# Performance work log

Measured on AMD Instinct MI355X. Metric: run time of the kernel, lower is better.

The kernel has to match this reference:

```python
import jax, jax.numpy as jnp
import numpy as np

K = 7        # upsample_kernel_size
S = 2        # upscale_factor
EK = K - 2   # encoder kernel size (5)


def conv2d(x, w, b, padding):
    out = jax.lax.conv_general_dilated(
        x, w, window_strides=(1, 1), padding=[(padding, padding), (padding, padding)],
        dimension_numbers=('NCHW', 'OIHW', 'NCHW'))
    return out + b[None, :, None, None]


def pixel_shuffle(x, s):
    B, C, H, W = x.shape
    oc = C // (s * s)
    x = x.reshape(B, oc, s, s, H, W)
    x = x.transpose(0, 1, 4, 2, 5, 3)
    return x.reshape(B, oc, H * s, W * s)


def carafe(x, kmap, k, s):
    # x: [B,C,H,W], kmap: [B,k*k,H*s,W*s] softmax-normalized
    B, C, H, W = x.shape
    pad = k // 2
    xp = jnp.pad(x, ((0, 0), (0, 0), (pad, pad), (pad, pad)))
    # k^2 shifted views -> [B,C,k2,H,W]
    patches = jnp.stack([xp[:, :, dy:dy + H, dx:dx + W]
                         for dy in range(k) for dx in range(k)], axis=2)
    # output pixel (i,j) reads source (i//s, j//s): factor kmap spatial dims
    km = kmap.reshape(B, k * k, H, s, W, s)
    out = jnp.einsum('bcnhw,bnhpwq->bchpwq', patches, km)
    return out.reshape(B, C, H * s, W * s)


def setup_inputs() -> dict:
    key = jax.random.key(0)
    k1, k2, k3 = jax.random.split(key, 3)
    B, C, H, W = 4, 256, 64, 64
    comp_c = 64
    enc_out = (S * K) ** 2  # 196
    x = jax.random.normal(k1, (B, C, H, W), dtype=jnp.float32)
    w_comp = jax.random.normal(k2, (comp_c, C, 1, 1), dtype=jnp.float32) * (1.0 / np.sqrt(C))
    b_comp = jnp.zeros((comp_c,), dtype=jnp.float32)
    w_enc = jax.random.normal(k3, (enc_out, comp_c, EK, EK), dtype=jnp.float32) * (1.0 / np.sqrt(comp_c * EK * EK))
    b_enc = jnp.zeros((enc_out,), dtype=jnp.float32)
    return {'x': x, 'w_comp': w_comp, 'b_comp': b_comp, 'w_enc': w_enc, 'b_enc': b_enc}


def reference(x, w_comp, b_comp, w_enc, b_enc):
    compressed = conv2d(x, w_comp, b_comp, padding=0)
    content = conv2d(compressed, w_enc, b_enc, padding=EK // 2)
    upsampled = pixel_shuffle(content, S)            # [B, k^2, H*s, W*s]
    kernel_map = jax.nn.softmax(upsampled, axis=1)
    return carafe(x, kernel_map, K, S)
```

## Files before the change

### kernel.cpp

```cpp
#include <hip/hip_runtime.h>
#include <math.h>
#include <stdint.h>

#define B_   4
#define C_   256
#define H_   64
#define W_   64
#define CC_  64
#define OE_  196
#define OH_  128
#define OW_  128
#define XH_  72
#define NWB_ 10

typedef uint32_t u32;
typedef unsigned short u16;
typedef __attribute__((ext_vector_type(8))) short bf16x8;
typedef __attribute__((ext_vector_type(4))) float f32x4;
typedef __attribute__((ext_vector_type(4))) u32 u32x4;
typedef __attribute__((ext_vector_type(2))) u32 u32x2;

__device__ __forceinline__ u16 f2bf(float f) {
  u32 u = __builtin_bit_cast(u32, f);
  u32 r = (u + 0x7FFFu + ((u >> 16) & 1u)) >> 16;
  return (u16)r;
}

__global__ __launch_bounds__(256) void prep_weights(
    const float* __restrict__ w_comp, const float* __restrict__ w_enc,
    u16* __restrict__ wfrag, u16* __restrict__ wcf,
    u16* __restrict__ xw8) {
  int idx = blockIdx.x * 256 + threadIdx.x;
  if (idx < 50 * 14 * 64) {
    int lane = idx & 63;
    int mt   = (idx >> 6) % 14;
    int ks   = idx / (14 * 64);
    int o    = mt * 16 + (lane & 15);
    int tap  = ks >> 1, s = ks & 1;
    int ky   = tap / 5, kx = tap % 5;
    int cb   = s * 32 + (lane >> 4) * 8;
    u32 pk[4];
    #pragma unroll
    for (int p = 0; p < 4; ++p) {
      u16 lo = 0, hi = 0;
      if (o < OE_) {
        lo = f2bf(w_enc[((o * CC_ + cb + 2 * p) * 5 + ky) * 5 + kx]);
        hi = f2bf(w_enc[((o * CC_ + cb + 2 * p + 1) * 5 + ky) * 5 + kx]);
      }
      pk[p] = (u32)lo | ((u32)hi << 16);
    }
    *reinterpret_cast<u32x4*>(wfrag + (size_t)idx * 8) =
        *reinterpret_cast<u32x4*>(pk);
  }
  if (idx < 8 * 4 * 64) {
    int lane = idx & 63;
    int mt   = (idx >> 6) & 3;
    int ks   = idx >> 8;
    int o    = mt * 16 + (lane & 15);
    int cb   = ks * 32 + (lane >> 4) * 8;
    u32 pk[4];
    #pragma unroll
    for (int p = 0; p < 4; ++p) {
      u16 lo = f2bf(w_comp[o * C_ + cb + 2 * p]);
      u16 hi = f2bf(w_comp[o * C_ + cb + 2 * p + 1]);
      pk[p] = (u32)lo | ((u32)hi << 16);
    }
    *reinterpret_cast<u32x4*>(wcf + (size_t)idx * 8) =
        *reinterpret_cast<u32x4*>(pk);
  }
  {
    u32x4 z = {0, 0, 0, 0};
    for (int i = idx; i < 1088 * 256; i += 65536) {
      int zi = i >> 8, ck = i & 255;
      int b = zi / 272, r = zi % 272;
      int hp, wb;
      if (r < 30)      { hp = r / 10;             wb = r % 10; }
      else if (r < 80) { hp = 67 + (r - 30) / 10; wb = (r - 30) % 10; }
      else {
        int rr = r - 80;
        hp = 3 + rr / 3;
        int m = rr % 3;
        wb = (m == 0) ? 0 : (m == 1) ? 8 : 9;
      }
      *reinterpret_cast<u32x4*>(
          xw8 + (((size_t)(b * XH_ + hp)) * NWB_ + wb) * (C_ * 8) + ck * 8) = z;
    }
  }
}

__global__ __launch_bounds__(256) void compress_k(
    const float* __restrict__ x, const u16* __restrict__ wcf,
    const float* __restrict__ b_comp, u16* __restrict__ comp,
    u16* __restrict__ xw8) {
  __shared__ float xs[C_ * 20];
  int t   = threadIdx.x;
  int gid = blockIdx.x;
  int wq  = gid & 3;
  int bh  = gid >> 2;
  int b = bh >> 6, h = bh & 63;
  int w0 = wq * 16;

  const float* xrow = x + (size_t)b * C_ * H_ * W_ + (size_t)h * W_ + w0;
  for (int i = t; i < 1024; i += 256) {
    int c = i >> 2, q = i & 3;
    f32x4 v = *reinterpret_cast<const f32x4*>(xrow + (size_t)c * H_ * W_ + q * 4);
    *reinterpret_cast<f32x4*>(xs + c * 20 + q * 4) = v;
  }
  __syncthreads();

  int wv   = __builtin_amdgcn_readfirstlane(t >> 6);
  int lane = t & 63;
  int w    = lane & 15;
  int lg   = lane >> 4;

  bf16x8 af[8];
  #pragma unroll
  for (int ks = 0; ks < 8; ++ks)
    af[ks] = *reinterpret_cast<const bf16x8*>(
        wcf + (((size_t)ks * 4 + wv) * 64 + lane) * 8);

  f32x4 acc = {0.f, 0.f, 0.f, 0.f};
  #pragma unroll
  for (int ks = 0; ks < 8; ++ks) {
    short vv[8];
    #pragma unroll
    for (int j = 0; j < 8; ++j)
      vv[j] = (short)f2bf(xs[(ks * 32 + lg * 8 + j) * 20 + w]);
    bf16x8 bf = (bf16x8){vv[0], vv[1], vv[2], vv[3], vv[4], vv[5], vv[6], vv[7]};
    acc = __builtin_amdgcn_mfma_f32_16x16x32_bf16(af[ks], bf, acc, 0, 0, 0);
  }

  {
    int cc0 = wv * 16 + lg * 4;
    f32x4 bias = *reinterpret_cast<const f32x4*>(b_comp + cc0);
    u32 p0 = (u32)f2bf(acc[0] + bias[0]) | ((u32)f2bf(acc[1] + bias[1]) << 16);
    u32 p1 = (u32)f2bf(acc[2] + bias[2]) | ((u32)f2bf(acc[3] + bias[3]) << 16);
    u32x2 pk = {p0, p1};
    *reinterpret_cast<u32x2*>(comp + ((size_t)bh * 64 + w0 + w) * CC_ + cc0) = pk;
  }

  {
    int ww = t & 15, cq = t >> 4;
    int wp = w0 + ww + 3;
    size_t base = (((size_t)(b * XH_ + h + 3)) * NWB_ + (wp >> 3)) * (C_ * 8) + (wp & 7);
    #pragma unroll
    for (int i = 0; i < 16; ++i) {
      int c = cq * 16 + i;
      xw8[base + c * 8] = f2bf(xs[c * 20 + ww]);
    }
  }
}

#define ELG_ 32256

__device__ __forceinline__ void enc_lda(
    bf16x8 (&a)[2], const u16* __restrict__ wfrag,
    int ks, int mtbase, int lane) {
  #pragma unroll
  for (int mm = 0; mm < 2; ++mm)
    a[mm] = *reinterpret_cast<const bf16x8*>(
        wfrag + (((size_t)ks * 14 + mtbase + mm) * 64 + lane) * 8);
}

__device__ __forceinline__ void enc_step(
    int ks, const char* lds, const bf16x8 (&a)[2], f32x4 (&acc)[2][2],
    int nlane, int kq) {
  int tap = ks >> 1, s = ks & 1;
  int ky = tap / 5, kx = tap % 5;
  bf16x8 bf[2];
  #pragma unroll
  for (int nt = 0; nt < 2; ++nt) {
    int col = nt * 16 + nlane + kx;
    int byte = (((ky * 36 + col) * 64 + s * 32 + kq * 8) * 2) ^ ((col & 7) << 4);
    bf[nt] = *reinterpret_cast<const bf16x8*>(lds + byte);
  }
  #pragma unroll
  for (int mm = 0; mm < 2; ++mm)
    #pragma unroll
    for (int nt = 0; nt < 2; ++nt)
      acc[mm][nt] = __builtin_amdgcn_mfma_f32_16x16x32_bf16(
          a[mm], bf[nt], acc[mm][nt], 0, 0, 0);
}

__global__ __launch_bounds__(512) void enc_mfma_k(
    const u16* __restrict__ comp, const u16* __restrict__ wfrag,
    const float* __restrict__ b_enc, u16* __restrict__ bfrB) {
  __shared__ __align__(16) char lds[ELG_];

  int t   = threadIdx.x;
  int bid = blockIdx.x;
  int swz = (bid & 7) * 64 + (bid >> 3);
  int wh  = swz & 1;
  int bh  = swz >> 1;
  int b = bh >> 6, h = bh & 63;
  int w0 = wh * 32;

  {
    const u16* cbse = comp + (size_t)b * H_ * W_ * CC_;
    for (int i = t; i < 1440; i += 512) {
      int q = i & 7, colr = i >> 3;
      int col = colr % 36, r = colr / 36;
      int hh = h - 2 + r, gw = w0 - 2 + col;
      u32x4 v = {0, 0, 0, 0};
      if ((unsigned)hh < H_ && (unsigned)gw < W_)
        v = *reinterpret_cast<const u32x4*>(cbse + ((size_t)hh * W_ + gw) * CC_ + q * 8);
      int byte = ((r * 36 + col) * 128 + q * 16) ^ ((col & 7) << 4);
      *reinterpret_cast<u32x4*>(lds + byte) = v;
    }
  }
  __syncthreads();

  int wv    = __builtin_amdgcn_readfirstlane(t >> 6);
  int lane  = t & 63;
  int nlane = lane & 15, kq = lane >> 4;
  int mtbase = wv * 2;

  f32x4 acc[2][2];
  #pragma unroll
  for (int mm = 0; mm < 2; ++mm)
    #pragma unroll
    for (int nt = 0; nt < 2; ++nt) acc[mm][nt] = (f32x4){0.f, 0.f, 0.f, 0.f};

  if (wv < 7) {
    bf16x8 abuf[4][2];
    #pragma unroll
    for (int p = 0; p < 4; ++p) enc_lda(abuf[p], wfrag, p, mtbase, lane);
    #pragma unroll
    for (int ks = 0; ks < 50; ++ks) {
      enc_step(ks, lds, abuf[ks & 3], acc, nlane, kq);
      if (ks < 46) enc_lda(abuf[ks & 3], wfrag, ks + 4, mtbase, lane);
    }
  }

  __syncthreads();
  float* lg = (float*)lds;
  if (wv < 7) {
    #pragma unroll
    for (int mm = 0; mm < 2; ++mm) {
      #pragma unroll
      for (int nt = 0; nt < 2; ++nt) {
        #pragma unroll
        for (int r = 0; r < 4; ++r) {
          int m  = (mtbase + mm) * 16 + kq * 4 + r;
          int px = nt * 16 + nlane;
          lg[m * 36 + px] = acc[mm][nt][r] + (m < OE_ ? b_enc[m] : 0.f);
        }
      }
    }
  }
  __syncthreads();

  float v[49];
  float inv = 0.f;
  if (t < 128) {
    int px = t & 31, rr = t >> 5;
    float mx = -1e30f;
    #pragma unroll
    for (int n = 0; n < 49; ++n) {
      v[n] = lg[(4 * n + rr) * 36 + px];
      mx = fmaxf(mx, v[n]);
    }
    float sum = 0.f;
    #pragma unroll
    for (int n = 0; n < 49; ++n) { v[n] = __expf(v[n] - mx); sum += v[n]; }
    inv = 1.f / sum;
  }
  __syncthreads();

  if (t < 128) {
    int px = t & 31, rr = t >> 5;
    u16* sva = (u16*)lds;
    int myo = (px * 4 + rr) * 49;
    #pragma unroll
    for (int n = 0; n < 49; ++n) sva[myo + n] = f2bf(v[n] * inv);

    int wi = px & 7, wg = wh * 4 + (px >> 3);
    int p = rr >> 1, q = rr & 1;
    size_t bb = ((((size_t)(b * 64 + h) * 8 + wg) * 2 + p) * 4) * 512 +
                (size_t)(wi * 2 + q) * 8;
    #pragma unroll
    for (int ks = 0; ks < 4; ++ks) {
      #pragma unroll
      for (int lg2 = 0; lg2 < 4; ++lg2) {
        u32 pk[4];
        #pragma unroll
        for (int jp = 0; jp < 4; ++jp) {
          u16 e[2];
          #pragma unroll
          for (int u = 0; u < 2; ++u) {
            int j  = jp * 2 + u;
            int k  = ks * 32 + lg2 * 8 + j;
            int dy = k >> 4, dxp = k & 15;
            int dx = dxp - wi;
            bool ok = (dy < 7) && (dx >= 0) && (dx < 7);
            int idx = ok ? (dy * 7 + dx) : 0;
            u16 s = sva[myo + idx];
            e[u] = ok ? s : (u16)0;
          }
          pk[jp] = (u32)e[0] | ((u32)e[1] << 16);
        }
        *reinterpret_cast<u32x4*>(bfrB + bb + (size_t)ks * 512 + lg2 * 128) =
            *reinterpret_cast<u32x4*>(pk);
      }
    }
  }
}

__device__ __forceinline__ void carafe_lda(
    bf16x8 (&buf)[4], const u16* __restrict__ xb,
    int c, int h, int wg, int lg) {
  #pragma unroll
  for (int ks = 0; ks < 4; ++ks) {
    int dy = ks * 2 + (lg >> 1);
    buf[ks] = *reinterpret_cast<const bf16x8*>(
        xb + (((size_t)(h + dy)) * NWB_ + wg + (lg & 1)) * (C_ * 8) + c * 8);
  }
}

__global__ __launch_bounds__(256) void carafe_k(
    const u16* __restrict__ xw8, const u16* __restrict__ bfrB,
    float* __restrict__ out) {
  int t   = threadIdx.x;
  int bid = blockIdx.x;
  int swz = (bid & 7) * 256 + (bid >> 3);
  int mh  = swz & 1;
  int wgp = (swz >> 1) & 3;
  int h   = (swz >> 3) & 63;
  int b   = swz >> 9;

  int wv   = t >> 6;
  int lane = t & 63;
  int wg   = wgp * 2 + (wv & 1);
  int mq   = wv >> 1;
  int mt0  = mh * 8 + mq * 4;
  int col  = lane & 15;
  int lg   = lane >> 4;
  int mrow = lane & 15;
  int w0   = wg * 8;

  bf16x8 bfp[2][4];
  size_t bbase = (((size_t)(b * 64 + h) * 8 + wg) * 2) * 4 * 512;
  #pragma unroll
  for (int p = 0; p < 2; ++p)
    #pragma unroll
    for (int ks = 0; ks < 4; ++ks)
      bfp[p][ks] = *reinterpret_cast<const bf16x8*>(
          bfrB + bbase + (size_t)(p * 4 + ks) * 512 + lane * 8);

  const u16* xb = xw8 + (size_t)b * XH_ * NWB_ * (C_ * 8);
  bf16x8 bufA[4], bufB[4];
  carafe_lda(bufA, xb, mt0 * 16 + mrow, h, wg, lg);

  #pragma unroll
  for (int i = 0; i < 4; ++i) {
    int mt = mt0 + i;
    if (i < 3) {
      if (i & 1) carafe_lda(bufA, xb, (mt + 1) * 16 + mrow, h, wg, lg);
      else       carafe_lda(bufB, xb, (mt + 1) * 16 + mrow, h, wg, lg);
    }
    f32x4 acc0 = {0.f, 0.f, 0.f, 0.f};
    f32x4 acc1 = {0.f, 0.f, 0.f, 0.f};
    #pragma unroll
    for (int ks = 0; ks < 4; ++ks) {
      bf16x8 af = (i & 1) ? bufB[ks] : bufA[ks];
      acc0 = __builtin_amdgcn_mfma_f32_16x16x32_bf16(af, bfp[0][ks], acc0, 0, 0, 0);
      acc1 = __builtin_amdgcn_mfma_f32_16x16x32_bf16(af, bfp[1][ks], acc1, 0, 0, 0);
    }
    float* o0 = out +
        ((size_t)(b * C_ + mt * 16 + lg * 4) * OH_ + 2 * h) * OW_ + 2 * w0 + col;
    o0[0]                     = acc0[0];
    o0[(size_t)OH_ * OW_]     = acc0[1];
    o0[2 * (size_t)OH_ * OW_] = acc0[2];
    o0[3 * (size_t)OH_ * OW_] = acc0[3];
    float* o1 = o0 + OW_;
    o1[0]                     = acc1[0];
    o1[(size_t)OH_ * OW_]     = acc1[1];
    o1[2 * (size_t)OH_ * OW_] = acc1[2];
    o1[3 * (size_t)OH_ * OW_] = acc1[3];
  }
}

extern "C" void kernel_launch(void* const* d_in, const int* in_sizes, int n_in,
                              void* d_out, int out_size, void* d_ws, size_t ws_size,
                              hipStream_t stream) {
  const float* x      = (const float*)d_in[0];
  const float* w_comp = (const float*)d_in[1];
  const float* b_comp = (const float*)d_in[2];
  const float* w_enc  = (const float*)d_in[3];
  const float* b_enc  = (const float*)d_in[4];
  float* out = (float*)d_out;

  u16* bfrB  = (u16*)d_ws;
  u16* wfrag = bfrB + 8388608;
  u16* wcf   = wfrag + 358400;
  u16* comp  = wcf + 16384;
  u16* xw8   = comp + 1048576;

  prep_weights<<<256, 256, 0, stream>>>(w_comp, w_enc, wfrag, wcf, xw8);
  compress_k<<<B_ * H_ * 4, 256, 0, stream>>>(x, wcf, b_comp, comp, xw8);
  enc_mfma_k<<<512, 512, 0, stream>>>(comp, wfrag, b_enc, bfrB);
  carafe_k<<<2048, 256, 0, stream>>>(xw8, bfrB, out);
}
```

Baseline: 65.68 us.

## Realign compress blocks to 8-wide padded tiles and write xw8 with 16-byte stores

Compress blocks now cover a window shifted by the 3-pixel halo padding, so each block fills two whole 8-pixel groups of the padded bf16 x layout. Those groups are written with one 16-byte vector store per channel instead of 16 scattered 2-byte stores per thread. The side halo columns are written by the compress kernel itself (as zeros from the masked loads), which leaves prep_weights only the top and bottom rows to zero. The cost is one extra block per row (5 instead of 4), which recomputes some columns and masks their output, plus unaligned scalar LDS stores.

```diff
diff --git a/kernel.cpp b/kernel.cpp
--- a/kernel.cpp
+++ b/kernel.cpp
@@ -70,18 +70,11 @@
   }
   {
     u32x4 z = {0, 0, 0, 0};
-    for (int i = idx; i < 1088 * 256; i += 65536) {
-      int zi = i >> 8, ck = i & 255;
-      int b = zi / 272, r = zi % 272;
-      int hp, wb;
-      if (r < 30)      { hp = r / 10;             wb = r % 10; }
-      else if (r < 80) { hp = 67 + (r - 30) / 10; wb = (r - 30) % 10; }
-      else {
-        int rr = r - 80;
-        hp = 3 + rr / 3;
-        int m = rr % 3;
-        wb = (m == 0) ? 0 : (m == 1) ? 8 : 9;
-      }
+    for (int i = idx; i < 81920; i += 65536) {
+      int ck = i & 255, zi = i >> 8;
+      int b = zi / 80, r = zi % 80;
+      int hp8 = r / 10, wb = r % 10;
+      int hp = (hp8 < 3) ? hp8 : 64 + hp8;
       *reinterpret_cast<u32x4*>(
           xw8 + (((size_t)(b * XH_ + hp)) * NWB_ + wb) * (C_ * 8) + ck * 8) = z;
     }
@@ -92,25 +85,29 @@
     const float* __restrict__ x, const u16* __restrict__ wcf,
     const float* __restrict__ b_comp, u16* __restrict__ comp,
     u16* __restrict__ xw8) {
-  __shared__ float xs[C_ * 20];
+  __shared__ float xs[C_ * 25];
   int t   = threadIdx.x;
   int gid = blockIdx.x;
-  int wq  = gid & 3;
-  int bh  = gid >> 2;
+  int wq  = gid % 5;
+  int bh  = gid / 5;
   int b = bh >> 6, h = bh & 63;
-  int w0 = wq * 16;
-
-  const float* xrow = x + (size_t)b * C_ * H_ * W_ + (size_t)h * W_ + w0;
-  for (int i = t; i < 1024; i += 256) {
-    int c = i >> 2, q = i & 3;
-    f32x4 v = *reinterpret_cast<const f32x4*>(xrow + (size_t)c * H_ * W_ + q * 4);
-    *reinterpret_cast<f32x4*>(xs + c * 20 + q * 4) = v;
+  int wbase = wq * 16 - 4;
+
+  const float* xrow = x + (size_t)b * C_ * H_ * W_ + (size_t)h * W_;
+  for (int i = t; i < 1280; i += 256) {
+    int c = i / 5, q = i - (i / 5) * 5;
+    int gw0 = wbase + q * 4;
+    f32x4 v = {0.f, 0.f, 0.f, 0.f};
+    if ((unsigned)gw0 < 61u)
+      v = *reinterpret_cast<const f32x4*>(xrow + (size_t)c * H_ * W_ + gw0);
+    float* r = xs + c * 25 + q * 4;
+    r[0] = v[0]; r[1] = v[1]; r[2] = v[2]; r[3] = v[3];
   }
   __syncthreads();
 
   int wv   = __builtin_amdgcn_readfirstlane(t >> 6);
   int lane = t & 63;
-  int w    = lane & 15;
+  int i16  = lane & 15;
   int lg   = lane >> 4;
 
   bf16x8 af[8];
@@ -125,28 +122,38 @@
     short vv[8];
     #pragma unroll
     for (int j = 0; j < 8; ++j)
-      vv[j] = (short)f2bf(xs[(ks * 32 + lg * 8 + j) * 20 + w]);
+      vv[j] = (short)f2bf(xs[(ks * 32 + lg * 8 + j) * 25 + i16 + 1]);
     bf16x8 bf = (bf16x8){vv[0], vv[1], vv[2], vv[3], vv[4], vv[5], vv[6], vv[7]};
     acc = __builtin_amdgcn_mfma_f32_16x16x32_bf16(af[ks], bf, acc, 0, 0, 0);
   }
 
   {
-    int cc0 = wv * 16 + lg * 4;
-    f32x4 bias = *reinterpret_cast<const f32x4*>(b_comp + cc0);
-    u32 p0 = (u32)f2bf(acc[0] + bias[0]) | ((u32)f2bf(acc[1] + bias[1]) << 16);
-    u32 p1 = (u32)f2bf(acc[2] + bias[2]) | ((u32)f2bf(acc[3] + bias[3]) << 16);
-    u32x2 pk = {p0, p1};
-    *reinterpret_cast<u32x2*>(comp + ((size_t)bh * 64 + w0 + w) * CC_ + cc0) = pk;
+    int w = wq * 16 - 3 + i16;
+    if ((unsigned)w < (unsigned)W_) {
+      int cc0 = wv * 16 + lg * 4;
+      f32x4 bias = *reinterpret_cast<const f32x4*>(b_comp + cc0);
+      u32 p0 = (u32)f2bf(acc[0] + bias[0]) | ((u32)f2bf(acc[1] + bias[1]) << 16);
+      u32 p1 = (u32)f2bf(acc[2] + bias[2]) | ((u32)f2bf(acc[3] + bias[3]) << 16);
+      u32x2 pk = {p0, p1};
+      *reinterpret_cast<u32x2*>(comp + ((size_t)bh * 64 + w) * CC_ + cc0) = pk;
+    }
   }
 
   {
-    int ww = t & 15, cq = t >> 4;
-    int wp = w0 + ww + 3;
-    size_t base = (((size_t)(b * XH_ + h + 3)) * NWB_ + (wp >> 3)) * (C_ * 8) + (wp & 7);
-    #pragma unroll
-    for (int i = 0; i < 16; ++i) {
-      int c = cq * 16 + i;
-      xw8[base + c * 8] = f2bf(xs[c * 20 + ww]);
+    int c = t;
+    size_t row = ((size_t)(b * XH_ + h + 3)) * NWB_;
+    #pragma unroll
+    for (int g = 0; g < 2; ++g) {
+      int wb = wq * 2 + g;
+      u32 pk[4];
+      #pragma unroll
+      for (int jp = 0; jp < 4; ++jp) {
+        u16 lo = f2bf(xs[c * 25 + g * 8 + 1 + 2 * jp]);
+        u16 hi = f2bf(xs[c * 25 + g * 8 + 2 + 2 * jp]);
+        pk[jp] = (u32)lo | ((u32)hi << 16);
+      }
+      *reinterpret_cast<u32x4*>(xw8 + (row + wb) * (C_ * 8) + c * 8) =
+          *reinterpret_cast<u32x4*>(pk);
     }
   }
 }
@@ -397,7 +404,7 @@
   u16* xw8   = comp + 1048576;
 
   prep_weights<<<256, 256, 0, stream>>>(w_comp, w_enc, wfrag, wcf, xw8);
-  compress_k<<<B_ * H_ * 4, 256, 0, stream>>>(x, wcf, b_comp, comp, xw8);
+  compress_k<<<B_ * H_ * 5, 256, 0, stream>>>(x, wcf, b_comp, comp, xw8);
   enc_mfma_k<<<512, 512, 0, stream>>>(comp, wfrag, b_enc, bfrB);
   carafe_k<<<2048, 256, 0, stream>>>(xw8, bfrB, out);
 }
```

Result: faster. 64.02 us (-2.5%).
